# Optimization experiments

Hardware: AMD Instinct MI355X
Metric: run time of the kernel (lower is better)

Reference implementation:

```python
import jax, jax.numpy as jnp
import numpy as np

B, T, F_IN, SSL, D, H, L, P, FF = 16, 1024, 1024, 512, 256, 4, 4, 128, 2048
EPS = 1e-5


def layer_norm(x, w, b):
    m = x.mean(-1, keepdims=True)
    v = ((x - m) ** 2).mean(-1, keepdims=True)
    return (x - m) / jnp.sqrt(v + EPS) * w + b


def setup_inputs() -> dict:
    key = jax.random.key(0)
    ks = jax.random.split(key, 16)
    def w(k, shape, s=0.02):
        return jax.random.normal(k, shape, jnp.float32) * s
    inp = {}
    inp["features"] = jax.random.normal(ks[0], (B, T, F_IN), jnp.float32)
    inp["feat_lengths"] = jax.random.randint(ks[1], (B,), T // 2, T + 1)
    inp["phoneme_lengths"] = jax.random.randint(ks[2], (B, P), 1, 17)
    inp["ssl_W"] = w(ks[3], (SSL, F_IN)); inp["ssl_b"] = jnp.zeros((SSL,), jnp.float32)
    inp["ln0_w"] = jnp.ones((SSL,), jnp.float32); inp["ln0_b"] = jnp.zeros((SSL,), jnp.float32)
    inp["conv_W"] = w(ks[4], (D, SSL, 3)); inp["conv_b"] = jnp.zeros((D,), jnp.float32)
    inp["qkv_W"] = w(ks[5], (L, 3 * D, D)); inp["qkv_b"] = jnp.zeros((L, 3 * D), jnp.float32)
    inp["out_W"] = w(ks[6], (L, D, D)); inp["out_b"] = jnp.zeros((L, D), jnp.float32)
    inp["ln1_w"] = jnp.ones((L, D), jnp.float32); inp["ln1_b"] = jnp.zeros((L, D), jnp.float32)
    inp["ff1_W"] = w(ks[7], (L, FF, D)); inp["ff1_b"] = jnp.zeros((L, FF), jnp.float32)
    inp["ff2_W"] = w(ks[8], (L, D, FF)); inp["ff2_b"] = jnp.zeros((L, D), jnp.float32)
    inp["ln2_w"] = jnp.ones((L, D), jnp.float32); inp["ln2_b"] = jnp.zeros((L, D), jnp.float32)
    inp["fs1_W"] = w(ks[9], (D, D)); inp["fs1_b"] = jnp.zeros((D,), jnp.float32)
    inp["fs2_W"] = w(ks[10], (1, D)); inp["fs2_b"] = jnp.zeros((1,), jnp.float32)
    return inp


def reference(features, feat_lengths, phoneme_lengths, ssl_W, ssl_b, ln0_w, ln0_b,
              conv_W, conv_b, qkv_W, qkv_b, out_W, out_b, ln1_w, ln1_b,
              ff1_W, ff1_b, ff2_W, ff2_b, ln2_w, ln2_b, fs1_W, fs1_b, fs2_W, fs2_b):
    # SSL encoder: Linear -> ReLU -> (Dropout eval) -> LayerNorm
    x = jax.nn.relu(features @ ssl_W.T + ssl_b)
    x = layer_norm(x, ln0_w, ln0_b)
    # Conv1d k=3 pad=1 over time, then ReLU
    xc = jnp.transpose(x, (0, 2, 1))  # (B, SSL, T)
    xc = jax.lax.conv_general_dilated(xc, conv_W, (1,), ((1, 1),),
                                      dimension_numbers=("NCH", "OIH", "NCH"))
    xc = xc + conv_b[None, :, None]
    x = jax.nn.relu(jnp.transpose(xc, (0, 2, 1)))  # (B, T, D)

    mask = jnp.arange(T)[None, :] < feat_lengths[:, None]  # (B, T) valid frames
    hd = D // H
    scale = 1.0 / np.sqrt(hd).astype(np.float32)
    # Post-norm TransformerEncoderLayer (PyTorch default), ReLU FFN
    for l in range(L):
        qkv = x @ qkv_W[l].T + qkv_b[l]
        q, k, v = jnp.split(qkv, 3, axis=-1)
        q = q.reshape(B, T, H, hd); k = k.reshape(B, T, H, hd); v = v.reshape(B, T, H, hd)
        s = jnp.einsum("bqhd,bkhd->bhqk", q, k) * scale
        s = jnp.where(mask[:, None, None, :], s, -1e30)
        a = jax.nn.softmax(s, axis=-1)
        o = jnp.einsum("bhqk,bkhd->bqhd", a, v).reshape(B, T, D)
        x = layer_norm(x + o @ out_W[l].T + out_b[l], ln1_w[l], ln1_b[l])
        f = jax.nn.relu(x @ ff1_W[l].T + ff1_b[l]) @ ff2_W[l].T + ff2_b[l]
        x = layer_norm(x + f, ln2_w[l], ln2_b[l])

    fs = jax.nn.relu(x @ fs1_W.T + fs1_b) @ fs2_W.T + fs2_b  # (B, T, 1)
    frame_scores = jnp.where(mask, fs[..., 0], 0.0)

    # Vectorized segment mean (replaces per-element Python loop)
    valid = jnp.cumprod((phoneme_lengths > 0).astype(jnp.int32), axis=1)  # stop at first len<=0
    eff = phoneme_lengths * valid
    cum = jnp.cumsum(eff, axis=1)
    end = jnp.clip(cum, 0, T)
    start = jnp.clip(cum - eff, 0, T)
    cs = jnp.concatenate([jnp.zeros((B, 1), frame_scores.dtype),
                          jnp.cumsum(frame_scores, axis=1)], axis=1)  # (B, T+1)
    seg_sum = jnp.take_along_axis(cs, end, axis=1) - jnp.take_along_axis(cs, start, axis=1)
    cnt = end - start
    phoneme_scores = jnp.where(cnt > 0, seg_sum / jnp.maximum(cnt, 1), 0.0)

    pmask = phoneme_lengths > 0
    psum = (phoneme_scores * pmask).sum(axis=1)
    pcnt = jnp.maximum(pmask.sum(axis=1), 1)
    utterance_score = psum / pcnt
    pstd = jnp.sqrt((((phoneme_scores - utterance_score[:, None]) ** 2) * pmask).sum(axis=1) / pcnt)
    fluency_score = jnp.clip(100.0 - jnp.clip(pstd * 10.0, None, 100.0), 0.0, None)
    prosody_score = 0.5 * (utterance_score + fluency_score)
    return frame_scores, phoneme_scores, utterance_score, fluency_score, prosody_score
```

## Files before the change

kernel.cpp:

```cpp
#include <hip/hip_runtime.h>
#include <math.h>

#define B_   16
#define T_   1024
#define FIN_ 1024
#define SSL_ 512
#define D_   256
#define H_   4
#define HD_  64
#define L_   4
#define P_   128
#define FF_  2048
#define M_   (B_ * T_)
#define LN_EPS 1e-5f

typedef __attribute__((ext_vector_type(8))) short bf16x8;
typedef __attribute__((ext_vector_type(4))) float f32x4;

__device__ inline unsigned short f2bf(float f) {
    unsigned int u = __float_as_uint(f);
    u += 0x7fffu + ((u >> 16) & 1u);
    return (unsigned short)(u >> 16);
}
__device__ inline float bf2f(unsigned short h) {
    return __uint_as_float(((unsigned int)h) << 16);
}
__device__ inline bf16x8 pack8(float4 a, float4 b) {
    bf16x8 t;
    t[0] = (short)f2bf(a.x); t[1] = (short)f2bf(a.y);
    t[2] = (short)f2bf(a.z); t[3] = (short)f2bf(a.w);
    t[4] = (short)f2bf(b.x); t[5] = (short)f2bf(b.y);
    t[6] = (short)f2bf(b.z); t[7] = (short)f2bf(b.w);
    return t;
}
__device__ inline void glds16(const unsigned short* g, unsigned short* l) {
    __builtin_amdgcn_global_load_lds(
        (const __attribute__((address_space(1))) void*)g,
        (__attribute__((address_space(3))) void*)l, 16, 0, 0);
}

__global__ __launch_bounds__(256) void cvt_f2b(
    const float* __restrict__ s, unsigned short* __restrict__ d)
{
    size_t i = ((size_t)blockIdx.x * 256 + threadIdx.x) * 8;
    float4 a = *(const float4*)(s + i);
    float4 b = *(const float4*)(s + i + 4);
    *(bf16x8*)(d + i) = pack8(a, b);
}

__global__ __launch_bounds__(256) void cvt_convw(
    const float* __restrict__ s, unsigned short* __restrict__ d)
{
    int i = blockIdx.x * 256 + threadIdx.x;
    int kk = i >> 17, rem = i & 131071;
    int n = rem >> 9, c = rem & 511;
    d[i] = f2bf(s[(size_t)n * 1536 + c * 3 + kk]);
}

template <int RELU, int OBF>
__global__ __launch_bounds__(256) void gemm_ll(
    const unsigned short* __restrict__ Ab, const unsigned short* __restrict__ Wb,
    const float* __restrict__ bias, void* __restrict__ Cout,
    int Md, int Nd, int Kd)
{
    __shared__ __align__(16) unsigned short As[128 * 32];
    __shared__ __align__(16) unsigned short Bs[128 * 32];
    char* AsB = (char*)As;
    char* BsB = (char*)Bs;

    const int tid = threadIdx.x;
    const int m0 = blockIdx.y * 128, n0 = blockIdx.x * 128;
    const int w = tid >> 6, l = tid & 63;
    const int lr = l & 15, lg = l >> 4;
    const int wr = w >> 1, wc = w & 1;

    f32x4 acc[4][4];
#pragma unroll
    for (int mi = 0; mi < 4; ++mi)
#pragma unroll
        for (int ni = 0; ni < 4; ++ni) acc[mi][ni] = (f32x4){0.f, 0.f, 0.f, 0.f};

    int aoff[4], boff[4];
#pragma unroll
    for (int mi = 0; mi < 4; ++mi) {
        int row = wr * 64 + mi * 16 + lr;
        aoff[mi] = row * 64 + ((lg * 16) ^ (((row >> 1) & 3) << 4));
    }
#pragma unroll
    for (int ni = 0; ni < 4; ++ni) {
        int row = wc * 64 + ni * 16 + lr;
        boff[ni] = row * 64 + ((lg * 16) ^ (((row >> 1) & 3) << 4));
    }
    int srow[2], scp[2];
#pragma unroll
    for (int j = 0; j < 2; ++j) {
        int row = (w * 2 + j) * 16 + (l >> 2);
        srow[j] = row;
        scp[j] = (l & 3) ^ ((row >> 1) & 3);
    }

    for (int k0 = 0; k0 < Kd; k0 += 32) {
        __syncthreads();
#pragma unroll
        for (int j = 0; j < 2; ++j) {
            glds16(Ab + (size_t)(m0 + srow[j]) * Kd + k0 + scp[j] * 8,
                   As + (w * 2 + j) * 512);
            glds16(Wb + (size_t)(n0 + srow[j]) * Kd + k0 + scp[j] * 8,
                   Bs + (w * 2 + j) * 512);
        }
        __syncthreads();
        bf16x8 a[4], bb[4];
#pragma unroll
        for (int mi = 0; mi < 4; ++mi) a[mi] = *(bf16x8*)(AsB + aoff[mi]);
#pragma unroll
        for (int ni = 0; ni < 4; ++ni) bb[ni] = *(bf16x8*)(BsB + boff[ni]);
#pragma unroll
        for (int mi = 0; mi < 4; ++mi)
#pragma unroll
            for (int ni = 0; ni < 4; ++ni)
                acc[mi][ni] = __builtin_amdgcn_mfma_f32_16x16x32_bf16(
                    a[mi], bb[ni], acc[mi][ni], 0, 0, 0);
    }

#pragma unroll
    for (int ni = 0; ni < 4; ++ni) {
        int col = n0 + wc * 64 + ni * 16 + lr;
        float bj = bias[col];
#pragma unroll
        for (int mi = 0; mi < 4; ++mi) {
#pragma unroll
            for (int r = 0; r < 4; ++r) {
                int rowg = m0 + wr * 64 + mi * 16 + lg * 4 + r;
                float v = acc[mi][ni][r] + bj;
                if (RELU) v = fmaxf(v, 0.0f);
                if (OBF) {
                    ((unsigned short*)Cout)[(size_t)rowg * Nd + col] = f2bf(v);
                } else {
                    ((float*)Cout)[(size_t)rowg * Nd + col] = v;
                }
            }
        }
    }
}

__global__ __launch_bounds__(256) void conv_mfma(
    const unsigned short* __restrict__ xb, const unsigned short* __restrict__ wb,
    const float* __restrict__ cb, float* __restrict__ X,
    unsigned short* __restrict__ Xb)
{
    __shared__ __align__(16) unsigned short As[130 * 32];
    __shared__ __align__(16) unsigned short Bs[3 * 128 * 32];
    char* AsB = (char*)As;
    char* BsB = (char*)Bs;

    const int tid = threadIdx.x;
    const int n0 = blockIdx.x * 128, m0 = blockIdx.y * 128;
    const int t0 = m0 & 1023;
    const int w = tid >> 6, l = tid & 63;
    const int lr = l & 15, lg = l >> 4;
    const int wr = w >> 1, wc = w & 1;

    f32x4 acc[4][4];
#pragma unroll
    for (int mi = 0; mi < 4; ++mi)
#pragma unroll
        for (int ni = 0; ni < 4; ++ni) acc[mi][ni] = (f32x4){0.f, 0.f, 0.f, 0.f};

    int aoff[4][3], boff[4][3];
#pragma unroll
    for (int mi = 0; mi < 4; ++mi)
#pragma unroll
        for (int kk = 0; kk < 3; ++kk) {
            int row = wr * 64 + mi * 16 + lr + kk;
            aoff[mi][kk] = row * 64 + ((lg * 16) ^ (((row >> 1) & 3) << 4));
        }
#pragma unroll
    for (int ni = 0; ni < 4; ++ni) {
        int nl = wc * 64 + ni * 16 + lr;
#pragma unroll
        for (int kk = 0; kk < 3; ++kk)
            boff[ni][kk] = kk * 8192 + nl * 64 + ((lg * 16) ^ (((nl >> 1) & 3) << 4));
    }

    for (int c0 = 0; c0 < 512; c0 += 32) {
        __syncthreads();
#pragma unroll
        for (int it = 0; it < 3; ++it) {
            int id = tid + it * 256;
            if (id < 520) {
                int r = id >> 2, ch = id & 3;
                int t = t0 + r - 1;
                bf16x8 v = (bf16x8){0, 0, 0, 0, 0, 0, 0, 0};
                if ((unsigned)t < 1024u)
                    v = *(const bf16x8*)(xb + (size_t)(m0 + r - 1) * 512 + c0 + ch * 8);
                *(bf16x8*)(AsB + r * 64 + ((ch * 16) ^ (((r >> 1) & 3) << 4))) = v;
            }
        }
#pragma unroll
        for (int it = 0; it < 6; ++it) {
            int id = tid + it * 256;
            int kk = id >> 9, rem = id & 511;
            int nl = rem >> 2, ch = rem & 3;
            bf16x8 v = *(const bf16x8*)(wb + (size_t)kk * 131072 +
                                        (size_t)(n0 + nl) * 512 + c0 + ch * 8);
            *(bf16x8*)(BsB + kk * 8192 + nl * 64 +
                       ((ch * 16) ^ (((nl >> 1) & 3) << 4))) = v;
        }
        __syncthreads();
#pragma unroll
        for (int kk = 0; kk < 3; ++kk) {
            bf16x8 bb[4];
#pragma unroll
            for (int ni = 0; ni < 4; ++ni) bb[ni] = *(bf16x8*)(BsB + boff[ni][kk]);
#pragma unroll
            for (int mi = 0; mi < 4; ++mi) {
                bf16x8 a = *(bf16x8*)(AsB + aoff[mi][kk]);
#pragma unroll
                for (int ni = 0; ni < 4; ++ni)
                    acc[mi][ni] = __builtin_amdgcn_mfma_f32_16x16x32_bf16(
                        a, bb[ni], acc[mi][ni], 0, 0, 0);
            }
        }
    }

#pragma unroll
    for (int ni = 0; ni < 4; ++ni) {
        int col = n0 + wc * 64 + ni * 16 + lr;
        float bj = cb[col];
#pragma unroll
        for (int mi = 0; mi < 4; ++mi) {
#pragma unroll
            for (int r = 0; r < 4; ++r) {
                int m = m0 + wr * 64 + mi * 16 + lg * 4 + r;
                float v = fmaxf(acc[mi][ni][r] + bj, 0.0f);
                X[(size_t)m * 256 + col] = v;
                Xb[(size_t)m * 256 + col] = f2bf(v);
            }
        }
    }
}

__global__ __launch_bounds__(512) void attn_mfma(
    const unsigned short* __restrict__ qkvb, const int* __restrict__ lens,
    unsigned short* __restrict__ Ob)
{
    __shared__ __align__(16) unsigned short Kt[64 * 64];
    __shared__ __align__(16) unsigned short Vt[64 * 64];
    __shared__ __align__(16) unsigned short Pt[8][16 * 64];

    const int qt = blockIdx.x, h = blockIdx.y, b = blockIdx.z;
    const int tid = threadIdx.x;
    const int w = tid >> 6, l = tid & 63;
    const int lr = l & 15, lg = l >> 4;
    const int len = lens[b];
    const int nt = (len + 63) >> 6;
    const size_t base = (size_t)b * (T_ * 768);
    const int q0 = qt * 128 + w * 16;

    char* KtB = (char*)Kt;
    char* VtB = (char*)Vt;
    char* PtB = (char*)(Pt[w]);

    bf16x8 qf[2];
#pragma unroll
    for (int half = 0; half < 2; ++half)
        qf[half] = *(const bf16x8*)(qkvb + base + (size_t)(q0 + lr) * 768 +
                                    h * 64 + lg * 8 + half * 32);

    float mrun = -3e38f, lrun = 0.0f;
    f32x4 acc_o[4];
#pragma unroll
    for (int td = 0; td < 4; ++td) acc_o[td] = (f32x4){0.f, 0.f, 0.f, 0.f};

    const int skr = tid >> 3, skc = tid & 7;

    for (int tk = 0; tk < nt; ++tk) {
        const int kv0 = tk * 64;
        __syncthreads();
        {
            const unsigned short* kp =
                qkvb + base + (size_t)(kv0 + skr) * 768 + h * 64 + 256 + skc * 8;
            *(bf16x8*)(KtB + skr * 128 + ((skc << 4) ^ ((skr & 7) << 4))) =
                *(const bf16x8*)kp;
            bf16x8 vv = *(const bf16x8*)(kp + 256);
#pragma unroll
            for (int j = 0; j < 8; ++j) {
                int d = skc * 8 + j;
                *(unsigned short*)(VtB + d * 128 + ((skr * 2) ^ ((d & 7) << 4))) =
                    (unsigned short)vv[j];
            }
        }
        __syncthreads();

        f32x4 accs[4];
        __builtin_amdgcn_s_setprio(1);
#pragma unroll
        for (int kt = 0; kt < 4; ++kt) {
            int row = kt * 16 + lr;
            int rb = row * 128, sw = (row & 7) << 4;
            bf16x8 k0 = *(bf16x8*)(KtB + rb + ((lg * 16) ^ sw));
            bf16x8 k1 = *(bf16x8*)(KtB + rb + ((lg * 16 + 64) ^ sw));
            f32x4 z = (f32x4){0.f, 0.f, 0.f, 0.f};
            f32x4 t = __builtin_amdgcn_mfma_f32_16x16x32_bf16(k0, qf[0], z, 0, 0, 0);
            accs[kt] = __builtin_amdgcn_mfma_f32_16x16x32_bf16(k1, qf[1], t, 0, 0, 0);
        }
        __builtin_amdgcn_s_setprio(0);

        float p[16];
        float pmax = -3e38f;
#pragma unroll
        for (int kt = 0; kt < 4; ++kt)
#pragma unroll
            for (int r = 0; r < 4; ++r) {
                int kidx = kv0 + kt * 16 + lg * 4 + r;
                float v = (kidx < len) ? accs[kt][r] * 0.125f : -1e30f;
                p[kt * 4 + r] = v;
                pmax = fmaxf(pmax, v);
            }
        pmax = fmaxf(pmax, __shfl_xor(pmax, 16));
        pmax = fmaxf(pmax, __shfl_xor(pmax, 32));
        float mnew = fmaxf(mrun, pmax);
        float alpha = __expf(mrun - mnew);
        float psum = 0.0f;
#pragma unroll
        for (int i = 0; i < 16; ++i) {
            float e = __expf(p[i] - mnew);
            p[i] = e;
            psum += e;
        }
        psum += __shfl_xor(psum, 16);
        psum += __shfl_xor(psum, 32);
        lrun = lrun * alpha + psum;
        mrun = mnew;
#pragma unroll
        for (int td = 0; td < 4; ++td) acc_o[td] *= alpha;

        const int swq = (lr & 7) << 4;
#pragma unroll
        for (int kt = 0; kt < 4; ++kt) {
            unsigned int p01 = (unsigned int)f2bf(p[kt * 4 + 0]) |
                               ((unsigned int)f2bf(p[kt * 4 + 1]) << 16);
            unsigned int p23 = (unsigned int)f2bf(p[kt * 4 + 2]) |
                               ((unsigned int)f2bf(p[kt * 4 + 3]) << 16);
            uint2 pw; pw.x = p01; pw.y = p23;
            *(uint2*)(PtB + lr * 128 + ((kt * 32 + lg * 8) ^ swq)) = pw;
        }
        bf16x8 pf0 = *(bf16x8*)(PtB + lr * 128 + ((lg * 16) ^ swq));
        bf16x8 pf1 = *(bf16x8*)(PtB + lr * 128 + ((lg * 16 + 64) ^ swq));
        __builtin_amdgcn_s_setprio(1);
#pragma unroll
        for (int td = 0; td < 4; ++td) {
            int d = td * 16 + lr;
            int db = d * 128, swd = (d & 7) << 4;
            bf16x8 v0 = *(bf16x8*)(VtB + db + ((lg * 16) ^ swd));
            bf16x8 v1 = *(bf16x8*)(VtB + db + ((lg * 16 + 64) ^ swd));
            acc_o[td] = __builtin_amdgcn_mfma_f32_16x16x32_bf16(v0, pf0, acc_o[td], 0, 0, 0);
            acc_o[td] = __builtin_amdgcn_mfma_f32_16x16x32_bf16(v1, pf1, acc_o[td], 0, 0, 0);
        }
        __builtin_amdgcn_s_setprio(0);
    }

    float inv = 1.0f / lrun;
    const int tglob = q0 + lr;
#pragma unroll
    for (int td = 0; td < 4; ++td)
#pragma unroll
        for (int r = 0; r < 4; ++r) {
            int d = td * 16 + lg * 4 + r;
            Ob[((size_t)b * T_ + tglob) * 256 + h * 64 + d] = f2bf(acc_o[td][r] * inv);
        }
}

__global__ __launch_bounds__(256) void ln0_bf16(
    const unsigned short* __restrict__ xin, const float* __restrict__ w,
    const float* __restrict__ b, unsigned short* __restrict__ out)
{
    const int lane = threadIdx.x & 63;
    const int wv = threadIdx.x >> 6;
    const int row = blockIdx.x * 4 + wv;

    bf16x8 v8 = *(const bf16x8*)(xin + (size_t)row * 512 + lane * 8);
    float f[8];
    float s = 0.0f, sq = 0.0f;
#pragma unroll
    for (int j = 0; j < 8; ++j) {
        f[j] = bf2f((unsigned short)v8[j]);
        s += f[j];
        sq += f[j] * f[j];
    }
#pragma unroll
    for (int d = 1; d < 64; d <<= 1) {
        s += __shfl_xor(s, d);
        sq += __shfl_xor(sq, d);
    }
    float mean = s / 512.0f;
    float var = fmaxf(sq / 512.0f - mean * mean, 0.0f);
    float inv = 1.0f / sqrtf(var + LN_EPS);
    float4 w0 = *(const float4*)(w + lane * 8);
    float4 w1 = *(const float4*)(w + lane * 8 + 4);
    float4 b0 = *(const float4*)(b + lane * 8);
    float4 b1 = *(const float4*)(b + lane * 8 + 4);
    float wv8[8] = {w0.x, w0.y, w0.z, w0.w, w1.x, w1.y, w1.z, w1.w};
    float bv8[8] = {b0.x, b0.y, b0.z, b0.w, b1.x, b1.y, b1.z, b1.w};
    bf16x8 o;
#pragma unroll
    for (int j = 0; j < 8; ++j)
        o[j] = (short)f2bf((f[j] - mean) * inv * wv8[j] + bv8[j]);
    *(bf16x8*)(out + (size_t)row * 512 + lane * 8) = o;
}

__global__ __launch_bounds__(256) void ln_res_dual(
    const float* __restrict__ xin, const float* __restrict__ resid,
    const float* __restrict__ w, const float* __restrict__ b,
    float* __restrict__ out, unsigned short* __restrict__ outb)
{
    const int lane = threadIdx.x & 63;
    const int wv = threadIdx.x >> 6;
    const int row = blockIdx.x * 4 + wv;

    float4 t = *(const float4*)(xin + (size_t)row * 256 + lane * 4);
    float4 r4 = *(const float4*)(resid + (size_t)row * 256 + lane * 4);
    t.x += r4.x; t.y += r4.y; t.z += r4.z; t.w += r4.w;
    float s = t.x + t.y + t.z + t.w;
    float sq = t.x * t.x + t.y * t.y + t.z * t.z + t.w * t.w;
#pragma unroll
    for (int d = 1; d < 64; d <<= 1) {
        s += __shfl_xor(s, d);
        sq += __shfl_xor(sq, d);
    }
    float mean = s / 256.0f;
    float var = fmaxf(sq / 256.0f - mean * mean, 0.0f);
    float inv = 1.0f / sqrtf(var + LN_EPS);
    float4 wc = *(const float4*)(w + lane * 4);
    float4 bc = *(const float4*)(b + lane * 4);
    float4 o;
    o.x = (t.x - mean) * inv * wc.x + bc.x;
    o.y = (t.y - mean) * inv * wc.y + bc.y;
    o.z = (t.z - mean) * inv * wc.z + bc.z;
    o.w = (t.w - mean) * inv * wc.w + bc.w;
    *(float4*)(out + (size_t)row * 256 + lane * 4) = o;
    uint2 ob;
    ob.x = (unsigned int)f2bf(o.x) | ((unsigned int)f2bf(o.y) << 16);
    ob.y = (unsigned int)f2bf(o.z) | ((unsigned int)f2bf(o.w) << 16);
    *(uint2*)(outb + (size_t)row * 256 + lane * 4) = ob;
}

__global__ __launch_bounds__(256) void frame_score_kernel(
    const float* __restrict__ hbuf, const float* __restrict__ w2,
    const float* __restrict__ b2, const int* __restrict__ lens,
    float* __restrict__ frame_out)
{
    const int lane = threadIdx.x & 63;
    const int wv = threadIdx.x >> 6;
    const int rowm = blockIdx.x * 4 + wv;
    float4 hv = *(const float4*)(hbuf + (size_t)rowm * 256 + lane * 4);
    float4 w4 = *(const float4*)(w2 + lane * 4);
    float s = hv.x * w4.x + hv.y * w4.y + hv.z * w4.z + hv.w * w4.w;
#pragma unroll
    for (int d = 1; d < 64; d <<= 1) s += __shfl_xor(s, d);
    if (lane == 0) {
        int b = rowm >> 10, t = rowm & 1023;
        float fs = s + b2[0];
        frame_out[rowm] = (t < lens[b]) ? fs : 0.0f;
    }
}

__global__ __launch_bounds__(64) void phoneme_kernel(
    const float* __restrict__ frame, const int* __restrict__ plen,
    float* __restrict__ pscore, float* __restrict__ utt,
    float* __restrict__ flu, float* __restrict__ pros)
{
    __shared__ float cs[T_ + 1];
    __shared__ float ps[P_];
    __shared__ int pmk[P_];

    const int b = blockIdx.x;
    const int lane = threadIdx.x;

    float loc[16];
    float run = 0.0f;
#pragma unroll
    for (int i = 0; i < 16; ++i) {
        run += frame[(size_t)b * T_ + lane * 16 + i];
        loc[i] = run;
    }
    float lanesum = run;
    float incl = lanesum;
#pragma unroll
    for (int d = 1; d < 64; d <<= 1) {
        float y = __shfl_up(incl, d);
        if (lane >= d) incl += y;
    }
    float excl = incl - lanesum;
#pragma unroll
    for (int i = 0; i < 16; ++i) cs[lane * 16 + i + 1] = loc[i] + excl;
    if (lane == 0) cs[0] = 0.0f;
    __syncthreads();

    if (lane == 0) {
        int cum = 0, valid = 1;
        float psum = 0.0f;
        int pcnt = 0;
        for (int p = 0; p < P_; ++p) {
            int lp = plen[b * P_ + p];
            if (lp <= 0) valid = 0;
            int eff = valid ? lp : 0;
            int start = cum; if (start > T_) start = T_; if (start < 0) start = 0;
            cum += eff;
            int end = cum; if (end > T_) end = T_; if (end < 0) end = 0;
            int cnt = end - start;
            float score = (cnt > 0) ? (cs[end] - cs[start]) / (float)cnt : 0.0f;
            ps[p] = score;
            pmk[p] = (lp > 0) ? 1 : 0;
            if (lp > 0) { psum += score; pcnt += 1; }
            pscore[b * P_ + p] = score;
        }
        int pc = pcnt > 0 ? pcnt : 1;
        float u = psum / (float)pc;
        float vsum = 0.0f;
        for (int p = 0; p < P_; ++p) {
            float d = ps[p] - u;
            if (pmk[p]) vsum += d * d;
        }
        float pstd = sqrtf(vsum / (float)pc);
        float f = 100.0f - fminf(pstd * 10.0f, 100.0f);
        f = fmaxf(f, 0.0f);
        utt[b] = u;
        flu[b] = f;
        pros[b] = 0.5f * (u + f);
    }
}

extern "C" void kernel_launch(void* const* d_in, const int* in_sizes, int n_in,
                              void* d_out, int out_size, void* d_ws, size_t ws_size,
                              hipStream_t stream)
{
    const float* features = (const float*)d_in[0];
    const int* feat_len = (const int*)d_in[1];
    const int* plen = (const int*)d_in[2];
    const float* ssl_W = (const float*)d_in[3];
    const float* ssl_b = (const float*)d_in[4];
    const float* ln0_w = (const float*)d_in[5];
    const float* ln0_b = (const float*)d_in[6];
    const float* conv_W = (const float*)d_in[7];
    const float* conv_b = (const float*)d_in[8];
    const float* qkv_W = (const float*)d_in[9];
    const float* qkv_b = (const float*)d_in[10];
    const float* out_W = (const float*)d_in[11];
    const float* out_b = (const float*)d_in[12];
    const float* ln1_w = (const float*)d_in[13];
    const float* ln1_b = (const float*)d_in[14];
    const float* ff1_W = (const float*)d_in[15];
    const float* ff1_b = (const float*)d_in[16];
    const float* ff2_W = (const float*)d_in[17];
    const float* ff2_b = (const float*)d_in[18];
    const float* ln2_w = (const float*)d_in[19];
    const float* ln2_b = (const float*)d_in[20];
    const float* fs1_W = (const float*)d_in[21];
    const float* fs1_b = (const float*)d_in[22];
    const float* fs2_W = (const float*)d_in[23];
    const float* fs2_b = (const float*)d_in[24];

    char* base = (char*)d_ws;
    unsigned short* FFb = (unsigned short*)base;
    unsigned short* featb = FFb;
    unsigned short* QKVb = (unsigned short*)(base + (size_t)M_ * 2048 * 2);
    unsigned short* x512b = QKVb;
    float* X = (float*)(base + (size_t)M_ * 2048 * 2 + (size_t)M_ * 768 * 2);
    unsigned short* Xb = (unsigned short*)((char*)X + (size_t)M_ * 256 * 4);
    unsigned short* Ob = Xb + (size_t)M_ * 256;
    float* T1 = (float*)((char*)Ob + (size_t)M_ * 256 * 2);
    unsigned short* sslWb = (unsigned short*)((char*)T1 + (size_t)M_ * 256 * 4);
    unsigned short* convWb = sslWb + 512 * 1024;
    unsigned short* qkvWb = convWb + 3 * 256 * 512;
    unsigned short* outWb = qkvWb + (size_t)L_ * 768 * 256;
    unsigned short* ff1Wb = outWb + (size_t)L_ * 256 * 256;
    unsigned short* ff2Wb = ff1Wb + (size_t)L_ * 2048 * 256;
    unsigned short* fs1Wb = ff2Wb + (size_t)L_ * 256 * 2048;

    float* frame = (float*)d_out;
    float* pscore = frame + M_;
    float* uttp = pscore + B_ * P_;
    float* flup = uttp + B_;
    float* prosp = flup + B_;

    cvt_f2b<<<8192, 256, 0, stream>>>(features, featb);
    cvt_f2b<<<256, 256, 0, stream>>>(ssl_W, sslWb);
    cvt_convw<<<1536, 256, 0, stream>>>(conv_W, convWb);
    cvt_f2b<<<384, 256, 0, stream>>>(qkv_W, qkvWb);
    cvt_f2b<<<128, 256, 0, stream>>>(out_W, outWb);
    cvt_f2b<<<1024, 256, 0, stream>>>(ff1_W, ff1Wb);
    cvt_f2b<<<1024, 256, 0, stream>>>(ff2_W, ff2Wb);
    cvt_f2b<<<32, 256, 0, stream>>>(fs1_W, fs1Wb);

    gemm_ll<1, 1><<<dim3(SSL_ / 128, M_ / 128), 256, 0, stream>>>(
        featb, sslWb, ssl_b, x512b, M_, SSL_, FIN_);
    ln0_bf16<<<M_ / 4, 256, 0, stream>>>(x512b, ln0_w, ln0_b, x512b);

    conv_mfma<<<dim3(2, M_ / 128), 256, 0, stream>>>(x512b, convWb, conv_b, X, Xb);

    for (int l = 0; l < L_; ++l) {
        gemm_ll<0, 1><<<dim3(768 / 128, M_ / 128), 256, 0, stream>>>(
            Xb, qkvWb + (size_t)l * 768 * 256, qkv_b + l * 768, QKVb, M_, 768, 256);
        attn_mfma<<<dim3(8, H_, B_), 512, 0, stream>>>(QKVb, feat_len, Ob);
        gemm_ll<0, 0><<<dim3(256 / 128, M_ / 128), 256, 0, stream>>>(
            Ob, outWb + (size_t)l * 256 * 256, out_b + l * 256, T1, M_, 256, 256);
        ln_res_dual<<<M_ / 4, 256, 0, stream>>>(
            T1, X, ln1_w + l * 256, ln1_b + l * 256, X, Xb);
        gemm_ll<1, 1><<<dim3(FF_ / 128, M_ / 128), 256, 0, stream>>>(
            Xb, ff1Wb + (size_t)l * FF_ * 256, ff1_b + l * FF_, FFb, M_, FF_, 256);
        gemm_ll<0, 0><<<dim3(256 / 128, M_ / 128), 256, 0, stream>>>(
            FFb, ff2Wb + (size_t)l * 256 * FF_, ff2_b + l * 256, T1, M_, 256, FF_);
        ln_res_dual<<<M_ / 4, 256, 0, stream>>>(
            T1, X, ln2_w + l * 256, ln2_b + l * 256, X, Xb);
    }

    gemm_ll<1, 0><<<dim3(256 / 128, M_ / 128), 256, 0, stream>>>(
        Xb, fs1Wb, fs1_b, T1, M_, 256, 256);
    frame_score_kernel<<<M_ / 4, 256, 0, stream>>>(T1, fs2_W, fs2_b, feat_len, frame);

    phoneme_kernel<<<B_, 64, 0, stream>>>(frame, plen, pscore, uttp, flup, prosp);
}
```

Before: 979.3 us.

## Keep residual stream and intermediate GEMM outputs in bf16 instead of fp32

Result: faster. 933.6 us (-4.7%).

```diff
diff --git a/kernel.cpp b/kernel.cpp
--- a/kernel.cpp
+++ b/kernel.cpp
@@ -145,8 +145,7 @@
 
 __global__ __launch_bounds__(256) void conv_mfma(
     const unsigned short* __restrict__ xb, const unsigned short* __restrict__ wb,
-    const float* __restrict__ cb, float* __restrict__ X,
-    unsigned short* __restrict__ Xb)
+    const float* __restrict__ cb, unsigned short* __restrict__ Xb)
 {
     __shared__ __align__(16) unsigned short As[130 * 32];
     __shared__ __align__(16) unsigned short Bs[3 * 128 * 32];
@@ -233,7 +232,6 @@
             for (int r = 0; r < 4; ++r) {
                 int m = m0 + wr * 64 + mi * 16 + lg * 4 + r;
                 float v = fmaxf(acc[mi][ni][r] + bj, 0.0f);
-                X[(size_t)m * 256 + col] = v;
                 Xb[(size_t)m * 256 + col] = f2bf(v);
             }
         }
@@ -409,20 +407,26 @@
     *(bf16x8*)(out + (size_t)row * 512 + lane * 8) = o;
 }
 
-__global__ __launch_bounds__(256) void ln_res_dual(
-    const float* __restrict__ xin, const float* __restrict__ resid,
+__global__ __launch_bounds__(256) void ln_res_bf16(
+    const unsigned short* __restrict__ t1, const unsigned short* __restrict__ resid,
     const float* __restrict__ w, const float* __restrict__ b,
-    float* __restrict__ out, unsigned short* __restrict__ outb)
+    unsigned short* __restrict__ out)
 {
     const int lane = threadIdx.x & 63;
     const int wv = threadIdx.x >> 6;
     const int row = blockIdx.x * 4 + wv;
-
-    float4 t = *(const float4*)(xin + (size_t)row * 256 + lane * 4);
-    float4 r4 = *(const float4*)(resid + (size_t)row * 256 + lane * 4);
-    t.x += r4.x; t.y += r4.y; t.z += r4.z; t.w += r4.w;
-    float s = t.x + t.y + t.z + t.w;
-    float sq = t.x * t.x + t.y * t.y + t.z * t.z + t.w * t.w;
+    const size_t off = (size_t)row * 256 + lane * 4;
+
+    uint2 a2 = *(const uint2*)(t1 + off);
+    uint2 r2 = *(const uint2*)(resid + off);
+    float t[4];
+    t[0] = bf2f((unsigned short)(a2.x & 0xffff)) + bf2f((unsigned short)(r2.x & 0xffff));
+    t[1] = bf2f((unsigned short)(a2.x >> 16))   + bf2f((unsigned short)(r2.x >> 16));
+    t[2] = bf2f((unsigned short)(a2.y & 0xffff)) + bf2f((unsigned short)(r2.y & 0xffff));
+    t[3] = bf2f((unsigned short)(a2.y >> 16))   + bf2f((unsigned short)(r2.y >> 16));
+
+    float s = t[0] + t[1] + t[2] + t[3];
+    float sq = t[0] * t[0] + t[1] * t[1] + t[2] * t[2] + t[3] * t[3];
 #pragma unroll
     for (int d = 1; d < 64; d <<= 1) {
         s += __shfl_xor(s, d);
@@ -433,29 +437,30 @@
     float inv = 1.0f / sqrtf(var + LN_EPS);
     float4 wc = *(const float4*)(w + lane * 4);
     float4 bc = *(const float4*)(b + lane * 4);
-    float4 o;
-    o.x = (t.x - mean) * inv * wc.x + bc.x;
-    o.y = (t.y - mean) * inv * wc.y + bc.y;
-    o.z = (t.z - mean) * inv * wc.z + bc.z;
-    o.w = (t.w - mean) * inv * wc.w + bc.w;
-    *(float4*)(out + (size_t)row * 256 + lane * 4) = o;
+    float o0 = (t[0] - mean) * inv * wc.x + bc.x;
+    float o1 = (t[1] - mean) * inv * wc.y + bc.y;
+    float o2 = (t[2] - mean) * inv * wc.z + bc.z;
+    float o3 = (t[3] - mean) * inv * wc.w + bc.w;
     uint2 ob;
-    ob.x = (unsigned int)f2bf(o.x) | ((unsigned int)f2bf(o.y) << 16);
-    ob.y = (unsigned int)f2bf(o.z) | ((unsigned int)f2bf(o.w) << 16);
-    *(uint2*)(outb + (size_t)row * 256 + lane * 4) = ob;
+    ob.x = (unsigned int)f2bf(o0) | ((unsigned int)f2bf(o1) << 16);
+    ob.y = (unsigned int)f2bf(o2) | ((unsigned int)f2bf(o3) << 16);
+    *(uint2*)(out + off) = ob;
 }
 
 __global__ __launch_bounds__(256) void frame_score_kernel(
-    const float* __restrict__ hbuf, const float* __restrict__ w2,
+    const unsigned short* __restrict__ hbuf, const float* __restrict__ w2,
     const float* __restrict__ b2, const int* __restrict__ lens,
     float* __restrict__ frame_out)
 {
     const int lane = threadIdx.x & 63;
     const int wv = threadIdx.x >> 6;
     const int rowm = blockIdx.x * 4 + wv;
-    float4 hv = *(const float4*)(hbuf + (size_t)rowm * 256 + lane * 4);
+    uint2 h2 = *(const uint2*)(hbuf + (size_t)rowm * 256 + lane * 4);
     float4 w4 = *(const float4*)(w2 + lane * 4);
-    float s = hv.x * w4.x + hv.y * w4.y + hv.z * w4.z + hv.w * w4.w;
+    float s = bf2f((unsigned short)(h2.x & 0xffff)) * w4.x +
+              bf2f((unsigned short)(h2.x >> 16)) * w4.y +
+              bf2f((unsigned short)(h2.y & 0xffff)) * w4.z +
+              bf2f((unsigned short)(h2.y >> 16)) * w4.w;
 #pragma unroll
     for (int d = 1; d < 64; d <<= 1) s += __shfl_xor(s, d);
     if (lane == 0) {
@@ -566,11 +571,10 @@
     unsigned short* featb = FFb;
     unsigned short* QKVb = (unsigned short*)(base + (size_t)M_ * 2048 * 2);
     unsigned short* x512b = QKVb;
-    float* X = (float*)(base + (size_t)M_ * 2048 * 2 + (size_t)M_ * 768 * 2);
-    unsigned short* Xb = (unsigned short*)((char*)X + (size_t)M_ * 256 * 4);
+    unsigned short* Xb = (unsigned short*)((char*)QKVb + (size_t)M_ * 768 * 2);
     unsigned short* Ob = Xb + (size_t)M_ * 256;
-    float* T1 = (float*)((char*)Ob + (size_t)M_ * 256 * 2);
-    unsigned short* sslWb = (unsigned short*)((char*)T1 + (size_t)M_ * 256 * 4);
+    unsigned short* T1b = Ob + (size_t)M_ * 256;
+    unsigned short* sslWb = T1b + (size_t)M_ * 256;
     unsigned short* convWb = sslWb + 512 * 1024;
     unsigned short* qkvWb = convWb + 3 * 256 * 512;
     unsigned short* outWb = qkvWb + (size_t)L_ * 768 * 256;
@@ -597,27 +601,27 @@
         featb, sslWb, ssl_b, x512b, M_, SSL_, FIN_);
     ln0_bf16<<<M_ / 4, 256, 0, stream>>>(x512b, ln0_w, ln0_b, x512b);
 
-    conv_mfma<<<dim3(2, M_ / 128), 256, 0, stream>>>(x512b, convWb, conv_b, X, Xb);
+    conv_mfma<<<dim3(2, M_ / 128), 256, 0, stream>>>(x512b, convWb, conv_b, Xb);
 
     for (int l = 0; l < L_; ++l) {
         gemm_ll<0, 1><<<dim3(768 / 128, M_ / 128), 256, 0, stream>>>(
             Xb, qkvWb + (size_t)l * 768 * 256, qkv_b + l * 768, QKVb, M_, 768, 256);
         attn_mfma<<<dim3(8, H_, B_), 512, 0, stream>>>(QKVb, feat_len, Ob);
-        gemm_ll<0, 0><<<dim3(256 / 128, M_ / 128), 256, 0, stream>>>(
-            Ob, outWb + (size_t)l * 256 * 256, out_b + l * 256, T1, M_, 256, 256);
-        ln_res_dual<<<M_ / 4, 256, 0, stream>>>(
-            T1, X, ln1_w + l * 256, ln1_b + l * 256, X, Xb);
+        gemm_ll<0, 1><<<dim3(256 / 128, M_ / 128), 256, 0, stream>>>(
+            Ob, outWb + (size_t)l * 256 * 256, out_b + l * 256, T1b, M_, 256, 256);
+        ln_res_bf16<<<M_ / 4, 256, 0, stream>>>(
+            T1b, Xb, ln1_w + l * 256, ln1_b + l * 256, Xb);
         gemm_ll<1, 1><<<dim3(FF_ / 128, M_ / 128), 256, 0, stream>>>(
             Xb, ff1Wb + (size_t)l * FF_ * 256, ff1_b + l * FF_, FFb, M_, FF_, 256);
-        gemm_ll<0, 0><<<dim3(256 / 128, M_ / 128), 256, 0, stream>>>(
-            FFb, ff2Wb + (size_t)l * 256 * FF_, ff2_b + l * 256, T1, M_, 256, FF_);
-        ln_res_dual<<<M_ / 4, 256, 0, stream>>>(
-            T1, X, ln2_w + l * 256, ln2_b + l * 256, X, Xb);
-    }
-
-    gemm_ll<1, 0><<<dim3(256 / 128, M_ / 128), 256, 0, stream>>>(
-        Xb, fs1Wb, fs1_b, T1, M_, 256, 256);
-    frame_score_kernel<<<M_ / 4, 256, 0, stream>>>(T1, fs2_W, fs2_b, feat_len, frame);
+        gemm_ll<0, 1><<<dim3(256 / 128, M_ / 128), 256, 0, stream>>>(
+            FFb, ff2Wb + (size_t)l * 256 * FF_, ff2_b + l * 256, T1b, M_, 256, FF_);
+        ln_res_bf16<<<M_ / 4, 256, 0, stream>>>(
+            T1b, Xb, ln2_w + l * 256, ln2_b + l * 256, Xb);
+    }
+
+    gemm_ll<1, 1><<<dim3(256 / 128, M_ / 128), 256, 0, stream>>>(
+        Xb, fs1Wb, fs1_b, T1b, M_, 256, 256);
+    frame_score_kernel<<<M_ / 4, 256, 0, stream>>>(T1b, fs2_W, fs2_b, feat_len, frame);
 
     phoneme_kernel<<<B_, 64, 0, stream>>>(frame, plen, pscore, uttp, flup, prosp);
 }
```
